# Kernel optimization log

Hardware: AMD Instinct MI355X
Metric: run time of the kernel (lower is better)

## Reference

```python
import jax, jax.numpy as jnp
import numpy as np

PATCH = 3  # patch_size (init kwarg)
STRIDE = 1  # stride (init kwarg)
EPS_NORMALIZE = 1e-12  # F.normalize default eps
EPS_PATCH = 1e-5       # patch-norm eps in feature_match_index


def _unit_channels(feat):
    # F.normalize(feat.reshape(c,-1), dim=0): unit L2 norm over channels per pixel.
    n = jnp.linalg.norm(feat, axis=0, keepdims=True)
    return feat / jnp.maximum(n, EPS_NORMALIZE)


def _patches(feat, ps):
    # feat: (c, h, w) -> (c*ps*ps, n_patches) row-major over (h-ps+1, w-ps+1)
    c, h, w = feat.shape
    hp, wp = h - ps + 1, w - ps + 1
    cols = jnp.stack([feat[:, dy:dy + hp, dx:dx + wp]
                      for dy in range(ps) for dx in range(ps)], axis=1)  # (c, ps*ps, hp, wp)
    return cols.reshape(c * ps * ps, hp * wp)


def _per_item(fi, fr):
    # fi, fr: (c, h, w)
    c, h, w = fi.shape
    ps = PATCH
    hp, wp = h - ps + 1, w - ps + 1

    fi = _unit_channels(fi)
    fr = _unit_channels(fr)

    ref = _patches(fr, ps)                                   # (c*9, n_ref)
    ref = ref / (jnp.linalg.norm(ref, axis=0, keepdims=True) + EPS_PATCH)
    inp = _patches(fi, ps)                                   # (c*9, n_in)

    # Full cross-correlation cost volume (= chunked conv2d + running max in torch code)
    corr = jnp.einsum('ki,kr->ir', inp, ref)                 # (n_in, n_ref)
    max_idx = jnp.argmax(corr, axis=1).reshape(hp, wp)       # first occurrence on ties, same as torch running '>' max

    # index_to_flow
    flow_w = (max_idx % wp).astype(jnp.float32)
    flow_h = (max_idx // wp).astype(jnp.float32)
    grid_x = jnp.arange(wp, dtype=jnp.float32)[None, :]
    grid_y = jnp.arange(hp, dtype=jnp.float32)[:, None]
    flow = jnp.stack([flow_w - grid_x * jnp.ones((hp, wp), jnp.float32),
                      flow_h - grid_y * jnp.ones((hp, wp), jnp.float32)], axis=-1)  # (hp, wp, 2)
    flow = jnp.pad(flow, ((0, ps - 1), (0, ps - 1), (0, 0)))  # (h, w, 2)

    # tensor_shift for (i, j) in {0,1,2}^2, zero fill
    shifted = jnp.stack([jnp.pad(flow, ((i, 0), (j, 0), (0, 0)))[:h, :w]
                         for i in range(3) for j in range(3)], axis=0)  # (9, h, w, 2)
    return shifted


def setup_inputs() -> dict:
    key = jax.random.key(0)
    k1, k2 = jax.random.split(key)
    N, C, H, W = 2, 64, 96, 96
    return {
        'dense_features1': jax.random.normal(k1, (N, C, H, W), dtype=jnp.float32),
        'dense_features2': jax.random.normal(k2, (N, C, H, W), dtype=jnp.float32),
    }


def reference(dense_features1, dense_features2):
    shifted = jax.vmap(_per_item)(dense_features1, dense_features2)  # (N, 9, H, W, 2)
    N, _, H, W, _ = shifted.shape
    # pre_offset_reorder: even channels = flow_h (offset[...,1]), odd channels = flow_w (offset[...,0])
    out = jnp.stack([shifted[..., 1], shifted[..., 0]], axis=2).reshape(N, 18, H, W)
    return out
```

## Files before the change

### kernel.cpp

```cpp
#include <hip/hip_runtime.h>
#include <math.h>

static constexpr int NITEM = 2;
static constexpr int C = 64;
static constexpr int W = 96;
static constexpr int H = 96;
static constexpr int HW = H * W;
static constexpr int HP = 94;
static constexpr int NP = HP * HP;

static constexpr int PL = 8;
static constexpr int UNITS_PER_N = 1188;
static constexpr int NBLOCKS = 768;

__device__ __forceinline__ unsigned int fkey(float v) {
    unsigned int u = __float_as_uint(v);
    return (u & 0x80000000u) ? ~u : (u | 0x80000000u);
}

__global__ __launch_bounds__(256) void normalize_kernel(
    const float* __restrict__ f1, const float* __restrict__ f2,
    float2* __restrict__ fiP, float2* __restrict__ frP, float* __restrict__ ssn)
{
    int t = blockIdx.x * 256 + threadIdx.x;
    const int perTensor = NITEM * HW;
    if (t >= 2 * perTensor) return;
    int which = t / perTensor;
    int p = t - which * perTensor;
    int n = p / HW;
    int pix = p - n * HW;
    const float* src = (which ? f2 : f1) + (size_t)n * C * HW + pix;
    float s = 0.f;
    #pragma unroll
    for (int c = 0; c < C; c++) {
        float v = src[c * HW];
        s = fmaf(v, v, s);
    }
    float norm = sqrtf(s);
    float scale = 1.0f / fmaxf(norm, 1e-12f);
    int y = pix / W, x = pix - y * W;
    float2* base = (which ? frP : fiP) + ((size_t)n * H + y) * (32 * W) + x;
    #pragma unroll
    for (int c2 = 0; c2 < 32; c2++)
        base[c2 * W] = make_float2(src[(2 * c2) * HW] * scale,
                                   src[(2 * c2 + 1) * HW] * scale);
    if (which) ssn[p] = s * scale * scale;
}

__global__ __launch_bounds__(256) void refnorm_kernel(
    const float* __restrict__ ssn, float* __restrict__ invn)
{
    int t = blockIdx.x * 256 + threadIdx.x;
    if (t >= NITEM * NP) return;
    int n = t / NP;
    int r = t - n * NP;
    int yr = r / HP, xr = r - yr * HP;
    const float* s = ssn + n * HW;
    float acc = 0.f;
    #pragma unroll
    for (int dy = 0; dy < 3; dy++)
        #pragma unroll
        for (int dx = 0; dx < 3; dx++)
            acc += s[(yr + dy) * W + (xr + dx)];
    invn[t] = 1.0f / (sqrtf(acc) + 1e-5f);
}

__device__ __forceinline__ void stage_row(const void* gsrc, void* ldst, int lane, int wv)
{
#if defined(__has_builtin) && __has_builtin(__builtin_amdgcn_global_load_lds)
    const char* g = (const char*)gsrc;
    char* l = (char*)ldst;
    #pragma unroll
    for (int c = 0; c < 6; ++c) {
        const int off = wv * 6144 + c * 1024;
        __builtin_amdgcn_global_load_lds(
            (const __attribute__((address_space(1))) unsigned int*)(const void*)(g + off + lane * 16),
            (__attribute__((address_space(3))) unsigned int*)(void*)(l + off),
            16, 0, 0);
    }
#else
    const char* g = (const char*)gsrc;
    char* l = (char*)ldst;
    #pragma unroll
    for (int c = 0; c < 6; ++c) {
        const int off = wv * 6144 + c * 1024 + lane * 16;
        *(float4*)(l + off) = *(const float4*)(g + off);
    }
#endif
}

__global__ __launch_bounds__(256, 2) void corr_fused_kernel(
    const float2* __restrict__ fiP, const float2* __restrict__ frP,
    const float* __restrict__ invn, unsigned long long* __restrict__ best,
    unsigned int* __restrict__ tick)
{
    __shared__ struct {
        float2 Ap[32][96];
        float2 Bp[32][96];
        float  sh[3][2][100];
        int    sp;
    } sm;

    const int t = threadIdx.x;
    const int tu = t >> 4, tv = t & 15;
    const int lane = t & 63;
    const int quad = tu & 3;
    const int wv = t >> 6;
    const int u0 = 6 * tu, v0 = 6 * tv;
    const unsigned long long gmask = 0xFFFFull << (lane & 48);

    const int n = blockIdx.x & 1;

    const float2* fiPn = fiP + (size_t)n * H * (32 * W);
    const float2* frPn = frP + (size_t)n * H * (32 * W);
    const float* inv = invn + (size_t)n * NP;
    unsigned long long* bn = best + (size_t)n * NP;

    float pA[6][6], pB[6][6];

    for (;;) {
        if (t == 0) sm.sp = (int)atomicAdd(&tick[n * 16], 1u);
        __syncthreads();
        const int uj = sm.sp;
        if (uj >= UNITS_PER_N) break;

        int dy = 0, ya = 0, nb = 0;
        {
            int r = uj;
            for (int s = 0; s < 187; ++s) {
                int ady = (s + 1) >> 1;
                int nyi = 94 - ady;
                int q = (nyi + PL - 1) / PL;
                if (r < q) {
                    dy = (s & 1) ? -ady : ady;
                    ya = (dy < 0 ? -dy : 0) + r * PL;
                    nb = nyi - r * PL; if (nb > PL) nb = PL;
                    break;
                }
                r -= q;
            }
        }
        const int yb = ya + nb;

        stage_row(fiPn + (size_t)ya * (32 * W), &sm.Ap[0][0], lane, wv);
        stage_row(frPn + (size_t)(ya + dy) * (32 * W), &sm.Bp[0][0], lane, wv);
        asm volatile("s_waitcnt vmcnt(0)" ::: "memory");
        __syncthreads();

        for (int y = ya; y <= yb + 1; ++y) {
            const bool doLd = (y <= yb);
            const bool doFin = (y >= ya + 2);
            const bool doA = (y > ya);
            const int yi = y - 2;
            const int yr = yi + dy;

            float acc[6][6];
            #pragma unroll
            for (int i = 0; i < 6; ++i)
                #pragma unroll
                for (int jj = 0; jj < 6; ++jj) acc[i][jj] = 0.f;

            #pragma unroll 2
            for (int kp = 0; kp < 32; ++kp) {
                const float4* ap = (const float4*)&sm.Ap[kp][u0];
                const float4* bp = (const float4*)&sm.Bp[kp][v0];
                float4 a01 = ap[0], a23 = ap[1], a45 = ap[2];
                float4 b01 = bp[0], b23 = bp[1], b45 = bp[2];
                float ae[6] = {a01.x, a01.z, a23.x, a23.z, a45.x, a45.z};
                float ao[6] = {a01.y, a01.w, a23.y, a23.w, a45.y, a45.w};
                float be[6] = {b01.x, b01.z, b23.x, b23.z, b45.x, b45.z};
                float bo[6] = {b01.y, b01.w, b23.y, b23.w, b45.y, b45.w};
                #pragma unroll
                for (int i = 0; i < 6; ++i)
                    #pragma unroll
                    for (int jj = 0; jj < 6; ++jj) {
                        acc[i][jj] = fmaf(ae[i], be[jj], acc[i][jj]);
                        acc[i][jj] = fmaf(ao[i], bo[jj], acc[i][jj]);
                    }
            }

            if (quad == 0 && tu >= 4) {
                const int g = (tu >> 2) - 1;
                #pragma unroll
                for (int jj = 0; jj < 6; ++jj) {
                    sm.sh[g][0][v0 + jj] = acc[0][jj];
                    sm.sh[g][1][v0 + jj] = acc[1][jj];
                }
            }
            __syncthreads();

            if (doLd) {
                stage_row(fiPn + (size_t)(y + 1) * (32 * W), &sm.Ap[0][0], lane, wv);
                stage_row(frPn + (size_t)(y + 1 + dy) * (32 * W), &sm.Bp[0][0], lane, wv);
            }

            float c6[6], c7[6];
            #pragma unroll
            for (int i = 0; i < 6; ++i) {
                c6[i] = __shfl_down(acc[i][0], 1);
                c7[i] = __shfl_down(acc[i][1], 1);
            }
            float e6[8], e7[8];
            #pragma unroll
            for (int jj = 0; jj < 6; ++jj) {
                e6[jj] = __shfl_down(acc[0][jj], 16);
                e7[jj] = __shfl_down(acc[1][jj], 16);
            }
            e6[6] = __shfl_down(acc[0][0], 17);
            e6[7] = __shfl_down(acc[0][1], 17);
            e7[6] = __shfl_down(acc[1][0], 17);
            e7[7] = __shfl_down(acc[1][1], 17);
            if (quad == 3) {
                if (tu < 15) {
                    const int g = tu >> 2;
                    #pragma unroll
                    for (int jj = 0; jj < 8; ++jj) {
                        e6[jj] = sm.sh[g][0][v0 + jj];
                        e7[jj] = sm.sh[g][1][v0 + jj];
                    }
                } else {
                    #pragma unroll
                    for (int jj = 0; jj < 8; ++jj) { e6[jj] = 0.f; e7[jj] = 0.f; }
                }
            }

            float ivr[6];
            if (doFin) {
                const float* ivp = inv + (size_t)yr * HP;
                #pragma unroll
                for (int jj = 0; jj < 6; ++jj) {
                    int xr = v0 + jj;
                    ivr[jj] = ivp[xr > 93 ? 93 : xr];
                }
            }

            #pragma unroll
            for (int i = 0; i < 6; ++i) {
                float bv = -INFINITY; int bxr = 0;
                #pragma unroll
                for (int jj = 0; jj < 6; ++jj) {
                    const int i1 = (i + 1 <= 5) ? i + 1 : 0;
                    const int j1 = (jj + 1 <= 5) ? jj + 1 : 0;
                    const int i2 = (i + 2 <= 5) ? i + 2 : 0;
                    const int j2 = (jj + 2 <= 5) ? jj + 2 : 0;
                    float E0 = acc[i][jj];
                    float E1 = (i + 1 <= 5)
                             ? ((jj + 1 <= 5) ? acc[i1][j1] : c6[i1])
                             : e6[jj + 1];
                    float E2 = (i + 2 <= 5)
                             ? ((jj + 2 <= 5) ? acc[i2][j2]
                                              : ((jj + 2 == 6) ? c6[i2] : c7[i2]))
                             : ((i + 2 == 6) ? e6[jj + 2] : e7[jj + 2]);
                    float bx = (E0 + E1) + E2;
                    if (doFin) {
                        float v = (pA[i][jj] + bx) * ivr[jj];
                        int xr = v0 + jj;
                        if (xr < HP && (u0 + i) < HP && v > bv) { bv = v; bxr = xr; }
                    }
                    if (doA) pA[i][jj] = pB[i][jj] + bx;
                    pB[i][jj] = bx;
                }
                if (doFin) {
                    float mx = bv;
                    #pragma unroll
                    for (int m = 1; m < 16; m <<= 1)
                        mx = fmaxf(mx, __shfl_xor(mx, m));
                    unsigned long long ball = __ballot(bv == mx) & gmask;
                    int srcl = __ffsll(ball) - 1;
                    int wxr = __shfl(bxr, srcl);
                    if (tv == 0 && (u0 + i) < HP) {
                        unsigned long long key =
                            ((unsigned long long)fkey(mx) << 32)
                          | (unsigned int)(~(unsigned int)(yr * HP + wxr));
                        const size_t off = (size_t)yi * HP + (u0 + i);
                        if (key > bn[off]) atomicMax(&bn[off], key);
                    }
                }
            }

            if (doLd) asm volatile("s_waitcnt vmcnt(0)" ::: "memory");
            __syncthreads();
        }
    }
}

__global__ __launch_bounds__(256) void expand_best_kernel(
    const unsigned long long* __restrict__ best, float* __restrict__ out)
{
    int t = blockIdx.x * 256 + threadIdx.x;
    const int total = NITEM * 18 * HW;
    if (t >= total) return;
    int x = t % W;
    int y = (t / W) % H;
    int chn = (t / HW) % 18;
    int n = t / (18 * HW);
    int k = chn >> 1;
    int b = chn & 1;
    int is = k / 3, js = k - is * 3;
    int ys = y - is, xs = x - js;
    float val = 0.f;
    if (ys >= 0 && ys < HP && xs >= 0 && xs < HP) {
        int i = ys * HP + xs;
        unsigned long long key = best[(size_t)n * NP + i];
        int idx = (int)(~(unsigned int)key);
        int yr = idx / HP, xr = idx - yr * HP;
        val = b ? (float)(xr - xs) : (float)(yr - ys);
    }
    out[t] = val;
}

extern "C" void kernel_launch(void* const* d_in, const int* in_sizes, int n_in,
                              void* d_out, int out_size, void* d_ws, size_t ws_size,
                              hipStream_t stream) {
    (void)in_sizes; (void)n_in; (void)out_size; (void)ws_size;
    const float* f1 = (const float*)d_in[0];
    const float* f2 = (const float*)d_in[1];

    float2* fiP = (float2*)d_ws;
    float2* frP = fiP + (size_t)NITEM * H * 32 * W;
    float*  ssn = (float*)(frP + (size_t)NITEM * H * 32 * W);
    float*  invn = ssn + (size_t)NITEM * HW;
    unsigned long long* best =
        (unsigned long long*)((((uintptr_t)(invn + (size_t)NITEM * NP)) + 63) & ~(uintptr_t)63);
    unsigned int* tick = (unsigned int*)(best + (size_t)NITEM * NP);

    normalize_kernel<<<(2 * NITEM * HW + 255) / 256, 256, 0, stream>>>(f1, f2, fiP, frP, ssn);
    refnorm_kernel<<<(NITEM * NP + 255) / 256, 256, 0, stream>>>(ssn, invn);
    hipMemsetAsync(best, 0, (size_t)NITEM * NP * sizeof(unsigned long long) + 512, stream);
    corr_fused_kernel<<<NBLOCKS, 256, 0, stream>>>(fiP, frP, invn, best, tick);
    expand_best_kernel<<<(NITEM * 18 * HW + 255) / 256, 256, 0, stream>>>(best, (float*)d_out);
}
```

Baseline: 613.4 us.

## Halve LDS staging into two channel halves to raise occupancy and grid size

The per-row A/B LDS buffers are replaced by a single half-size slab holding 16 channel-pairs of each. The second half is loaded mid-row between two 16-step FMA loops, with extra barriers and waits. This cuts LDS per block so more blocks fit per CU, and the grid is raised from 768 to 1024 blocks to match. In exchange, each row now has an exposed, unoverlapped global-to-LDS load plus more synchronisation.

```diff
diff --git a/kernel.cpp b/kernel.cpp
--- a/kernel.cpp
+++ b/kernel.cpp
@@ -11,7 +11,7 @@
 
 static constexpr int PL = 8;
 static constexpr int UNITS_PER_N = 1188;
-static constexpr int NBLOCKS = 768;
+static constexpr int NBLOCKS = 1024;
 
 __device__ __forceinline__ unsigned int fkey(float v) {
     unsigned int u = __float_as_uint(v);
@@ -65,26 +65,25 @@
     invn[t] = 1.0f / (sqrtf(acc) + 1e-5f);
 }
 
-__device__ __forceinline__ void stage_row(const void* gsrc, void* ldst, int lane, int wv)
+__device__ __forceinline__ void stage_half(const char* aH, const char* bH,
+                                           char* slot, int wv, int lane)
 {
 #if defined(__has_builtin) && __has_builtin(__builtin_amdgcn_global_load_lds)
-    const char* g = (const char*)gsrc;
-    char* l = (char*)ldst;
     #pragma unroll
     for (int c = 0; c < 6; ++c) {
-        const int off = wv * 6144 + c * 1024;
+        const int off = (wv * 6 + c) << 10;
+        const char* g = ((off < 12288) ? (aH + off) : (bH + (off - 12288))) + lane * 16;
         __builtin_amdgcn_global_load_lds(
-            (const __attribute__((address_space(1))) unsigned int*)(const void*)(g + off + lane * 16),
-            (__attribute__((address_space(3))) unsigned int*)(void*)(l + off),
+            (const __attribute__((address_space(1))) unsigned int*)(const void*)g,
+            (__attribute__((address_space(3))) unsigned int*)(void*)(slot + off),
             16, 0, 0);
     }
 #else
-    const char* g = (const char*)gsrc;
-    char* l = (char*)ldst;
     #pragma unroll
     for (int c = 0; c < 6; ++c) {
-        const int off = wv * 6144 + c * 1024 + lane * 16;
-        *(float4*)(l + off) = *(const float4*)(g + off);
+        const int off = ((wv * 6 + c) << 10) + lane * 16;
+        const char* g = (off < 12288) ? (aH + off) : (bH + (off - 12288));
+        *(float4*)(slot + off) = *(const float4*)g;
     }
 #endif
 }
@@ -95,8 +94,7 @@
     unsigned int* __restrict__ tick)
 {
     __shared__ struct {
-        float2 Ap[32][96];
-        float2 Bp[32][96];
+        float2 slab[2][16][96];
         float  sh[3][2][100];
         int    sp;
     } sm;
@@ -142,17 +140,20 @@
         }
         const int yb = ya + nb;
 
-        stage_row(fiPn + (size_t)ya * (32 * W), &sm.Ap[0][0], lane, wv);
-        stage_row(frPn + (size_t)(ya + dy) * (32 * W), &sm.Bp[0][0], lane, wv);
-        asm volatile("s_waitcnt vmcnt(0)" ::: "memory");
-        __syncthreads();
+        stage_half((const char*)(fiPn + (size_t)ya * (32 * W)),
+                   (const char*)(frPn + (size_t)(ya + dy) * (32 * W)),
+                   (char*)&sm.slab[0][0][0], wv, lane);
 
         for (int y = ya; y <= yb + 1; ++y) {
-            const bool doLd = (y <= yb);
             const bool doFin = (y >= ya + 2);
             const bool doA = (y > ya);
             const int yi = y - 2;
             const int yr = yi + dy;
+            const char* rowA = (const char*)(fiPn + (size_t)y * (32 * W));
+            const char* rowB = (const char*)(frPn + (size_t)(y + dy) * (32 * W));
+
+            asm volatile("s_waitcnt vmcnt(0)" ::: "memory");
+            __syncthreads();
 
             float acc[6][6];
             #pragma unroll
@@ -161,9 +162,9 @@
                 for (int jj = 0; jj < 6; ++jj) acc[i][jj] = 0.f;
 
             #pragma unroll 2
-            for (int kp = 0; kp < 32; ++kp) {
-                const float4* ap = (const float4*)&sm.Ap[kp][u0];
-                const float4* bp = (const float4*)&sm.Bp[kp][v0];
+            for (int kp = 0; kp < 16; ++kp) {
+                const float4* ap = (const float4*)&sm.slab[0][kp][u0];
+                const float4* bp = (const float4*)&sm.slab[1][kp][v0];
                 float4 a01 = ap[0], a23 = ap[1], a45 = ap[2];
                 float4 b01 = bp[0], b23 = bp[1], b45 = bp[2];
                 float ae[6] = {a01.x, a01.z, a23.x, a23.z, a45.x, a45.z};
@@ -178,6 +179,30 @@
                         acc[i][jj] = fmaf(ao[i], bo[jj], acc[i][jj]);
                     }
             }
+            __syncthreads();
+            stage_half(rowA + 12288, rowB + 12288,
+                       (char*)&sm.slab[0][0][0], wv, lane);
+            asm volatile("s_waitcnt vmcnt(0)" ::: "memory");
+            __syncthreads();
+
+            #pragma unroll 2
+            for (int kp = 0; kp < 16; ++kp) {
+                const float4* ap = (const float4*)&sm.slab[0][kp][u0];
+                const float4* bp = (const float4*)&sm.slab[1][kp][v0];
+                float4 a01 = ap[0], a23 = ap[1], a45 = ap[2];
+                float4 b01 = bp[0], b23 = bp[1], b45 = bp[2];
+                float ae[6] = {a01.x, a01.z, a23.x, a23.z, a45.x, a45.z};
+                float ao[6] = {a01.y, a01.w, a23.y, a23.w, a45.y, a45.w};
+                float be[6] = {b01.x, b01.z, b23.x, b23.z, b45.x, b45.z};
+                float bo[6] = {b01.y, b01.w, b23.y, b23.w, b45.y, b45.w};
+                #pragma unroll
+                for (int i = 0; i < 6; ++i)
+                    #pragma unroll
+                    for (int jj = 0; jj < 6; ++jj) {
+                        acc[i][jj] = fmaf(ae[i], be[jj], acc[i][jj]);
+                        acc[i][jj] = fmaf(ao[i], bo[jj], acc[i][jj]);
+                    }
+            }
 
             if (quad == 0 && tu >= 4) {
                 const int g = (tu >> 2) - 1;
@@ -189,10 +214,10 @@
             }
             __syncthreads();
 
-            if (doLd) {
-                stage_row(fiPn + (size_t)(y + 1) * (32 * W), &sm.Ap[0][0], lane, wv);
-                stage_row(frPn + (size_t)(y + 1 + dy) * (32 * W), &sm.Bp[0][0], lane, wv);
-            }
+            if (y < yb + 1)
+                stage_half((const char*)(fiPn + (size_t)(y + 1) * (32 * W)),
+                           (const char*)(frPn + (size_t)(y + 1 + dy) * (32 * W)),
+                           (char*)&sm.slab[0][0][0], wv, lane);
 
             float c6[6], c7[6];
             #pragma unroll
@@ -277,9 +302,6 @@
                     }
                 }
             }
-
-            if (doLd) asm volatile("s_waitcnt vmcnt(0)" ::: "memory");
-            __syncthreads();
         }
     }
 }
```

Result: slower. 626.6 us (+2.1%).
